# Kernel optimization log

Hardware: AMD Instinct MI355X
Metric: run time of the kernel (lower is better)

The kernel has to match this reference:

```python
import jax, jax.numpy as jnp
import numpy as np
from jax import lax

B, C, P = 8, 32, 256      # batch, channels, patch side
KB = 2                    # buf_region = kernel_size - stride = 3 - 1
R_MASK = 1                # output_bypassing: last-column patch, r = small_padding = 1


def setup_inputs() -> dict:
    key = jax.random.key(0)
    ks = jax.random.split(key, 5)
    x = jax.random.normal(ks[0], (B, C, P, P), jnp.float32)
    # right-halo stored by the left-neighbor patch (store_right -> last 2 cols)
    rbuf = jax.random.normal(ks[1], (B, C, P, KB), jnp.float32)
    # bottom-halo stored by the top-neighbor patch AFTER its hcat (width P+2)
    bbuf = jax.random.normal(ks[2], (B, C, KB, P + KB), jnp.float32)
    W = jax.random.normal(ks[3], (C, C, 3, 3), jnp.float32) * 0.05
    bias = jax.random.normal(ks[4], (C,), jnp.float32) * 0.05
    return {"x": x, "rbuf": rbuf, "bbuf": bbuf, "W": W, "bias": bias}


def reference(x, rbuf, bbuf, W, bias):
    # output_bypassing: zero the rightmost R_MASK columns (image right edge)
    x = x.at[:, :, :, -R_MASK:].set(0.0)
    # hcat: prepend right-halo from left neighbor -> [B,C,P,P+2]
    x = jnp.concatenate([rbuf, x], axis=-1)
    # vcat: prepend bottom-halo from top neighbor -> [B,C,P+2,P+2]
    x = jnp.concatenate([bbuf, x], axis=-2)
    # (store_bot side effect omitted: pure function returns conv output only)
    out = lax.conv_general_dilated(
        x, W, window_strides=(1, 1), padding='VALID',
        dimension_numbers=('NCHW', 'OIHW', 'NCHW'))  # -> [B,C,P,P]
    return out + bias[None, :, None, None]
```

## Files before the change

kernel.cpp:

```cpp
#include <hip/hip_runtime.h>
#include <cstdint>


constexpr int B  = 8;
constexpr int C  = 32;
constexpr int P  = 256;
constexpr int KB = 2;
constexpr int TH = 16;
constexpr int TW = 32;
constexpr int RS = 34;
constexpr int PL = 612;
constexpr int XSZ = 16 * PL;

typedef short bf16x8 __attribute__((ext_vector_type(8)));
typedef float f32x4  __attribute__((ext_vector_type(4)));
union Frag { uint32_t u[4]; bf16x8 v; };

static __device__ __forceinline__ uint32_t pk_bf16(float lo, float hi) {
    uint32_t a  = __builtin_bit_cast(uint32_t, lo);
    uint32_t b2 = __builtin_bit_cast(uint32_t, hi);
    a  += 0x7FFFu + ((a  >> 16) & 1u);
    b2 += 0x7FFFu + ((b2 >> 16) & 1u);
    return (a >> 16) | (b2 & 0xFFFF0000u);
}

__global__ __launch_bounds__(256) void pack_w_kernel(
    const float* __restrict__ W, uint32_t* __restrict__ wpk)
{
    const int g = blockIdx.x * 256 + threadIdx.x;
    const float4 v = ((const float4*)W)[g];
    const float vv[4] = { v.x, v.y, v.z, v.w };
    uint16_t* wh = (uint16_t*)wpk;
    #pragma unroll
    for (int e = 0; e < 4; ++e) {
        const int flat = 4 * g + e;
        const int t    = flat % 9;
        const int rest = flat / 9;
        const int ic   = rest & 31;
        const int oc   = rest >> 5;
        const uint32_t u = __builtin_bit_cast(uint32_t, vv[e]);
        const uint16_t h = (uint16_t)((u + 0x7FFFu + ((u >> 16) & 1u)) >> 16);
        wh[(t * 512 + oc * 16 + (ic >> 1)) * 2 + (ic & 1)] = h;
    }
}

struct StP {
    float4 a0, a1, c0, c1;
    float  h0l, h0h, h1l, h1h;
};

__global__ __launch_bounds__(256, 2) void conv_mfma(
    const float* __restrict__ x,
    const float* __restrict__ rbuf,
    const float* __restrict__ bbuf,
    const uint32_t* __restrict__ wpk,
    const float* __restrict__ bias,
    float* __restrict__ out)
{
    const int tid  = threadIdx.x;
    const int lane = tid & 63;
    const int w    = tid >> 6;
    const int q    = lane >> 4;
    const int n16  = lane & 15;

    const int swz = (blockIdx.x & 7) * 128 + (blockIdx.x >> 3);
    const int cx = swz & 7, ty = (swz >> 3) & 15, b = swz >> 7;
    const int x0 = cx * TW, y0 = ty * TH;

    __shared__ uint32_t Xs[XSZ];

    const int srow = lane >> 2;
    const int scol = (lane & 3) * 8;
    const bool zc  = (x0 == P - TW) && ((lane & 3) == 3);

    const float* xb = x    + (size_t)b * C * P * P;
    const float* rb = rbuf + (size_t)b * C * P * KB;
    const float* bb = bbuf + (size_t)b * C * KB * (P + KB);
    const float* basep[3] = { xb, rb, bb };
    const int    psz[3]   = { P * P, P * KB, KB * (P + KB) };

    int h_ldso[2], h_ps[2];
    const float* h_bp[2];
    bool h_z[2];
    #pragma unroll
    for (int ci = 0; ci < 2; ++ci) {
        const int c = lane + 64 * ci;
        int prow, pcol;
        if (c < 68) { const int hr = (c >= 34) ? 1 : 0; prow = hr; pcol = c - 34 * hr; }
        else        { const int cc = c - 68; prow = KB + (cc >> 1); pcol = cc & 1; }
        h_ldso[ci] = prow * RS + pcol;
        const int gr = y0 + prow, gc = x0 + pcol;
        int sel, off; bool z = false;
        if (gr < KB)      { sel = 2; off = gr * (P + KB) + gc; }
        else if (gc < KB) { sel = 1; off = (gr - KB) * KB + gc; }
        else              { sel = 0; off = (gr - KB) * P + (gc - KB); z = (gc == P + KB - 1); }
        h_bp[ci] = basep[sel] + off;
        h_ps[ci] = psz[sel];
        h_z[ci]  = z;
    }
    const bool h1a = lane < 36;

    StP S[4];
    #pragma unroll
    for (int k2 = 0; k2 < 4; ++k2) {
        const int m = 4 * k2 + w;
        const float* pi = xb + (size_t)(2 * m) * (P * P) + (y0 + srow) * P + x0 + scol;
        S[k2].a0 = *(const float4*)pi;
        S[k2].a1 = *(const float4*)(pi + 4);
        S[k2].c0 = *(const float4*)(pi + P * P);
        S[k2].c1 = *(const float4*)(pi + P * P + 4);
        const float* p0 = h_bp[0] + (size_t)(2 * m) * h_ps[0];
        S[k2].h0l = h_z[0] ? 0.f : p0[0];
        S[k2].h0h = h_z[0] ? 0.f : p0[h_ps[0]];
        if (h1a) {
            const float* p1 = h_bp[1] + (size_t)(2 * m) * h_ps[1];
            S[k2].h1l = h_z[1] ? 0.f : p1[0];
            S[k2].h1h = h_z[1] ? 0.f : p1[h_ps[1]];
        }
    }

    #pragma unroll
    for (int k2 = 0; k2 < 4; ++k2) {
        const int m = 4 * k2 + w;
        float4 a1 = S[k2].a1, c1 = S[k2].c1;
        if (zc) { a1.w = 0.f; c1.w = 0.f; }
        uint2 p0, p1, p2, p3;
        p0.x = pk_bf16(S[k2].a0.x, S[k2].c0.x); p0.y = pk_bf16(S[k2].a0.y, S[k2].c0.y);
        p1.x = pk_bf16(S[k2].a0.z, S[k2].c0.z); p1.y = pk_bf16(S[k2].a0.w, S[k2].c0.w);
        p2.x = pk_bf16(a1.x, c1.x);             p2.y = pk_bf16(a1.y, c1.y);
        p3.x = pk_bf16(a1.z, c1.z);             p3.y = pk_bf16(a1.w, c1.w);
        uint32_t* base = Xs + m * PL + (srow + KB) * RS + KB + scol;
        *(uint2*)(base + 0) = p0;
        *(uint2*)(base + 2) = p1;
        *(uint2*)(base + 4) = p2;
        *(uint2*)(base + 6) = p3;
        Xs[m * PL + h_ldso[0]] = pk_bf16(S[k2].h0l, S[k2].h0h);
        if (h1a) Xs[m * PL + h_ldso[1]] = pk_bf16(S[k2].h1l, S[k2].h1h);
    }

    Frag Bf[9][2];
    #pragma unroll
    for (int t = 0; t < 9; ++t)
        #pragma unroll
        for (int oh = 0; oh < 2; ++oh)
            *(uint4*)Bf[t][oh].u =
                *(const uint4*)&wpk[t * 512 + (oh * 16 + n16) * 16 + q * 4];
    const float bv0 = bias[n16];
    const float bv1 = bias[16 + n16];

    __syncthreads();

    #pragma unroll
    for (int ch = 0; ch < 2; ++ch) {
        f32x4 acc[4][2];
        #pragma unroll
        for (int rr = 0; rr < 4; ++rr)
            #pragma unroll
            for (int oh = 0; oh < 2; ++oh)
                #pragma unroll
                for (int e = 0; e < 4; ++e) acc[rr][oh][e] = 0.f;

        #pragma unroll
        for (int dr = 0; dr < 6; ++dr) {
            Frag A[3];
            const uint32_t* ap = Xs + (4 * q) * PL + (4 * w + dr) * RS + 16 * ch + n16;
            #pragma unroll
            for (int kx = 0; kx < 3; ++kx)
                #pragma unroll
                for (int p = 0; p < 4; ++p)
                    A[kx].u[p] = ap[p * PL + kx];
            #pragma unroll
            for (int ky = 0; ky < 3; ++ky) {
                const int rr = dr - ky;
                if (rr >= 0 && rr < 4) {
                    #pragma unroll
                    for (int kx = 0; kx < 3; ++kx) {
                        acc[rr][0] = __builtin_amdgcn_mfma_f32_16x16x32_bf16(
                                         A[kx].v, Bf[ky * 3 + kx][0].v, acc[rr][0], 0, 0, 0);
                        acc[rr][1] = __builtin_amdgcn_mfma_f32_16x16x32_bf16(
                                         A[kx].v, Bf[ky * 3 + kx][1].v, acc[rr][1], 0, 0, 0);
                    }
                }
            }
        }

        #pragma unroll
        for (int oh = 0; oh < 2; ++oh) {
            const int oc = oh * 16 + n16;
            const float bv = oh ? bv1 : bv0;
            #pragma unroll
            for (int rr = 0; rr < 4; ++rr) {
                float4 v;
                v.x = acc[rr][oh][0] + bv;
                v.y = acc[rr][oh][1] + bv;
                v.z = acc[rr][oh][2] + bv;
                v.w = acc[rr][oh][3] + bv;
                *(float4*)&out[((size_t)(b * C + oc) * P + (y0 + 4 * w + rr)) * P
                               + x0 + 16 * ch + 4 * q] = v;
            }
        }
    }
}

extern "C" void kernel_launch(void* const* d_in, const int* in_sizes, int n_in,
                              void* d_out, int out_size, void* d_ws, size_t ws_size,
                              hipStream_t stream) {
    const float* x    = (const float*)d_in[0];
    const float* rbuf = (const float*)d_in[1];
    const float* bbuf = (const float*)d_in[2];
    const float* W    = (const float*)d_in[3];
    const float* bias = (const float*)d_in[4];
    float* out = (float*)d_out;
    uint32_t* wpk = (uint32_t*)d_ws;

    pack_w_kernel<<<9, 256, 0, stream>>>(W, wpk);
    conv_mfma<<<1024, 256, 0, stream>>>(x, rbuf, bbuf, wpk, bias, out);
}
```

Before: 133.6 us.

## Process two column tiles per block, prefetching second tile during first's MFMA

Each block now handles two horizontally adjacent 32-wide tiles instead of one, halving the grid to 512 blocks. Global loads for the second tile are issued into registers while MFMAs for the first tile run, then staged into shared memory after a barrier. This targets exposed global-load latency and amortizes the weight-fragment loads per block. In exchange it raises register pressure from holding a second staging set and leaves fewer blocks to spread across CUs.

After: 141.6 us. 1.06x slower.

```diff
diff --git a/kernel.cpp b/kernel.cpp
--- a/kernel.cpp
+++ b/kernel.cpp
@@ -63,15 +63,28 @@
     const int q    = lane >> 4;
     const int n16  = lane & 15;
 
-    const int swz = (blockIdx.x & 7) * 128 + (blockIdx.x >> 3);
-    const int cx = swz & 7, ty = (swz >> 3) & 15, b = swz >> 7;
-    const int x0 = cx * TW, y0 = ty * TH;
+    const int sw  = (blockIdx.x & 7) * 64 + (blockIdx.x >> 3);
+    const int b   = sw >> 6;
+    const int ty  = (sw >> 2) & 15;
+    const int cx0 = 2 * (sw & 3);
+    const int x00 = cx0 * TW, x01 = x00 + TW, y0 = ty * TH;
 
     __shared__ uint32_t Xs[XSZ];
 
     const int srow = lane >> 2;
     const int scol = (lane & 3) * 8;
-    const bool zc  = (x0 == P - TW) && ((lane & 3) == 3);
+
+    int prowA[2], pcolA[2], h_ldso[2];
+    #pragma unroll
+    for (int ci = 0; ci < 2; ++ci) {
+        const int c = lane + 64 * ci;
+        int prow, pcol;
+        if (c < 68) { const int hr = (c >= 34) ? 1 : 0; prow = hr; pcol = c - 34 * hr; }
+        else        { const int cc = c - 68; prow = KB + (cc >> 1); pcol = cc & 1; }
+        prowA[ci] = prow; pcolA[ci] = pcol;
+        h_ldso[ci] = prow * RS + pcol;
+    }
+    const bool h1a = lane < 36;
 
     const float* xb = x    + (size_t)b * C * P * P;
     const float* rb = rbuf + (size_t)b * C * P * KB;
@@ -79,64 +92,54 @@
     const float* basep[3] = { xb, rb, bb };
     const int    psz[3]   = { P * P, P * KB, KB * (P + KB) };
 
-    int h_ldso[2], h_ps[2];
-    const float* h_bp[2];
-    bool h_z[2];
-    #pragma unroll
-    for (int ci = 0; ci < 2; ++ci) {
-        const int c = lane + 64 * ci;
-        int prow, pcol;
-        if (c < 68) { const int hr = (c >= 34) ? 1 : 0; prow = hr; pcol = c - 34 * hr; }
-        else        { const int cc = c - 68; prow = KB + (cc >> 1); pcol = cc & 1; }
-        h_ldso[ci] = prow * RS + pcol;
-        const int gr = y0 + prow, gc = x0 + pcol;
-        int sel, off; bool z = false;
-        if (gr < KB)      { sel = 2; off = gr * (P + KB) + gc; }
-        else if (gc < KB) { sel = 1; off = (gr - KB) * KB + gc; }
-        else              { sel = 0; off = (gr - KB) * P + (gc - KB); z = (gc == P + KB - 1); }
-        h_bp[ci] = basep[sel] + off;
-        h_ps[ci] = psz[sel];
-        h_z[ci]  = z;
-    }
-    const bool h1a = lane < 36;
-
-    StP S[4];
-    #pragma unroll
-    for (int k2 = 0; k2 < 4; ++k2) {
-        const int m = 4 * k2 + w;
+    auto mkh = [&](int x0, const float** bp, int* ps, bool* z) {
+        #pragma unroll
+        for (int ci = 0; ci < 2; ++ci) {
+            const int gr = y0 + prowA[ci], gc = x0 + pcolA[ci];
+            int sel, off; bool zz = false;
+            if (gr < KB)      { sel = 2; off = gr * (P + KB) + gc; }
+            else if (gc < KB) { sel = 1; off = (gr - KB) * KB + gc; }
+            else              { sel = 0; off = (gr - KB) * P + (gc - KB);
+                                zz = (gc == P + KB - 1); }
+            bp[ci] = basep[sel] + off;
+            ps[ci] = psz[sel];
+            z[ci]  = zz;
+        }
+    };
+
+    auto ldp = [&](int m, int x0, const float* const* bp, const int* ps,
+                   const bool* z, StP& S) {
         const float* pi = xb + (size_t)(2 * m) * (P * P) + (y0 + srow) * P + x0 + scol;
-        S[k2].a0 = *(const float4*)pi;
-        S[k2].a1 = *(const float4*)(pi + 4);
-        S[k2].c0 = *(const float4*)(pi + P * P);
-        S[k2].c1 = *(const float4*)(pi + P * P + 4);
-        const float* p0 = h_bp[0] + (size_t)(2 * m) * h_ps[0];
-        S[k2].h0l = h_z[0] ? 0.f : p0[0];
-        S[k2].h0h = h_z[0] ? 0.f : p0[h_ps[0]];
+        S.a0 = *(const float4*)pi;
+        S.a1 = *(const float4*)(pi + 4);
+        S.c0 = *(const float4*)(pi + P * P);
+        S.c1 = *(const float4*)(pi + P * P + 4);
+        const float* p0 = bp[0] + (size_t)(2 * m) * ps[0];
+        S.h0l = z[0] ? 0.f : p0[0];
+        S.h0h = z[0] ? 0.f : p0[ps[0]];
         if (h1a) {
-            const float* p1 = h_bp[1] + (size_t)(2 * m) * h_ps[1];
-            S[k2].h1l = h_z[1] ? 0.f : p1[0];
-            S[k2].h1h = h_z[1] ? 0.f : p1[h_ps[1]];
-        }
-    }
-
-    #pragma unroll
-    for (int k2 = 0; k2 < 4; ++k2) {
-        const int m = 4 * k2 + w;
-        float4 a1 = S[k2].a1, c1 = S[k2].c1;
-        if (zc) { a1.w = 0.f; c1.w = 0.f; }
+            const float* p1 = bp[1] + (size_t)(2 * m) * ps[1];
+            S.h1l = z[1] ? 0.f : p1[0];
+            S.h1h = z[1] ? 0.f : p1[ps[1]];
+        }
+    };
+
+    auto stp = [&](int m, const StP& S, bool zcc) {
+        float4 a1 = S.a1, c1 = S.c1;
+        if (zcc) { a1.w = 0.f; c1.w = 0.f; }
         uint2 p0, p1, p2, p3;
-        p0.x = pk_bf16(S[k2].a0.x, S[k2].c0.x); p0.y = pk_bf16(S[k2].a0.y, S[k2].c0.y);
-        p1.x = pk_bf16(S[k2].a0.z, S[k2].c0.z); p1.y = pk_bf16(S[k2].a0.w, S[k2].c0.w);
-        p2.x = pk_bf16(a1.x, c1.x);             p2.y = pk_bf16(a1.y, c1.y);
-        p3.x = pk_bf16(a1.z, c1.z);             p3.y = pk_bf16(a1.w, c1.w);
+        p0.x = pk_bf16(S.a0.x, S.c0.x); p0.y = pk_bf16(S.a0.y, S.c0.y);
+        p1.x = pk_bf16(S.a0.z, S.c0.z); p1.y = pk_bf16(S.a0.w, S.c0.w);
+        p2.x = pk_bf16(a1.x, c1.x);     p2.y = pk_bf16(a1.y, c1.y);
+        p3.x = pk_bf16(a1.z, c1.z);     p3.y = pk_bf16(a1.w, c1.w);
         uint32_t* base = Xs + m * PL + (srow + KB) * RS + KB + scol;
         *(uint2*)(base + 0) = p0;
         *(uint2*)(base + 2) = p1;
         *(uint2*)(base + 4) = p2;
         *(uint2*)(base + 6) = p3;
-        Xs[m * PL + h_ldso[0]] = pk_bf16(S[k2].h0l, S[k2].h0h);
-        if (h1a) Xs[m * PL + h_ldso[1]] = pk_bf16(S[k2].h1l, S[k2].h1h);
-    }
+        Xs[m * PL + h_ldso[0]] = pk_bf16(S.h0l, S.h0h);
+        if (h1a) Xs[m * PL + h_ldso[1]] = pk_bf16(S.h1l, S.h1h);
+    };
 
     Frag Bf[9][2];
     #pragma unroll
@@ -148,10 +151,7 @@
     const float bv0 = bias[n16];
     const float bv1 = bias[16 + n16];
 
-    __syncthreads();
-
-    #pragma unroll
-    for (int ch = 0; ch < 2; ++ch) {
+    auto mfma_ch = [&](int ch, int x0) {
         f32x4 acc[4][2];
         #pragma unroll
         for (int rr = 0; rr < 4; ++rr)
@@ -183,7 +183,6 @@
                 }
             }
         }
-
         #pragma unroll
         for (int oh = 0; oh < 2; ++oh) {
             const int oc = oh * 16 + n16;
@@ -199,7 +198,38 @@
                                + x0 + 16 * ch + 4 * q] = v;
             }
         }
-    }
+    };
+
+    const float* bp0[2]; int ps0[2]; bool z0[2];
+    mkh(x00, bp0, ps0, z0);
+    StP S0[4];
+    #pragma unroll
+    for (int k2 = 0; k2 < 4; ++k2) ldp(4 * k2 + w, x00, bp0, ps0, z0, S0[k2]);
+    #pragma unroll
+    for (int k2 = 0; k2 < 4; ++k2) stp(4 * k2 + w, S0[k2], false);
+    __syncthreads();
+
+    const float* bp1[2]; int ps1[2]; bool z1[2];
+    mkh(x01, bp1, ps1, z1);
+    const bool zc1 = (x01 == P - TW) && ((lane & 3) == 3);
+    StP S1[4];
+    ldp(w,     x01, bp1, ps1, z1, S1[0]);
+    ldp(4 + w, x01, bp1, ps1, z1, S1[1]);
+
+    mfma_ch(0, x00);
+
+    ldp(8 + w,  x01, bp1, ps1, z1, S1[2]);
+    ldp(12 + w, x01, bp1, ps1, z1, S1[3]);
+
+    mfma_ch(1, x00);
+    __syncthreads();
+
+    #pragma unroll
+    for (int k2 = 0; k2 < 4; ++k2) stp(4 * k2 + w, S1[k2], zc1);
+    __syncthreads();
+
+    mfma_ch(0, x01);
+    mfma_ch(1, x01);
 }
 
 extern "C" void kernel_launch(void* const* d_in, const int* in_sizes, int n_in,
@@ -214,5 +244,5 @@
     uint32_t* wpk = (uint32_t*)d_ws;
 
     pack_w_kernel<<<9, 256, 0, stream>>>(W, wpk);
-    conv_mfma<<<1024, 256, 0, stream>>>(x, rbuf, bbuf, wpk, bias, out);
-}
+    conv_mfma<<<512, 256, 0, stream>>>(x, rbuf, bbuf, wpk, bias, out);
+}
```
